# Optimization experiments

Hardware: AMD Instinct MI355X
Metric: run time of the kernel (lower is better)

## Reference

```python
import jax, jax.numpy as jnp
import numpy as np

OBS_DIM, GOAL_DIM, NUM_SKILLS, ACTION_DIM = 256, 64, 16, 32
HIDDEN = 128
BATCH = 65536


def setup_inputs() -> dict:
    key = jax.random.key(0)
    ks = jax.random.split(key, 10)
    s = lambda k, shape, fan_in: jax.random.normal(k, shape, jnp.float32) * (1.0 / np.sqrt(fan_in))
    return {
        "obs": jax.random.normal(ks[0], (BATCH, OBS_DIM), jnp.float32),
        "goals": jax.random.normal(ks[1], (BATCH, GOAL_DIM), jnp.float32),
        # gate (AlphaNet) params
        "Wa1": s(ks[2], (OBS_DIM + GOAL_DIM, HIDDEN), OBS_DIM + GOAL_DIM),
        "ba1": jnp.zeros((HIDDEN,), jnp.float32),
        "Wa2": s(ks[3], (HIDDEN, NUM_SKILLS), HIDDEN),
        "ba2": jnp.zeros((NUM_SKILLS,), jnp.float32),
        # stacked executor params: [S, in, out]
        "W1": s(ks[4], (NUM_SKILLS, OBS_DIM, HIDDEN), OBS_DIM),
        "b1": jnp.zeros((NUM_SKILLS, HIDDEN), jnp.float32),
        "W2": s(ks[5], (NUM_SKILLS, HIDDEN, ACTION_DIM), HIDDEN),
        "b2": jnp.zeros((NUM_SKILLS, ACTION_DIM), jnp.float32),
    }


def reference(obs, goals, Wa1, ba1, Wa2, ba2, W1, b1, W2, b2):
    # gate: softmax(Linear(ReLU(Linear(cat(obs, goals)))))
    concat_input = jnp.concatenate([obs, goals], axis=-1)  # [B, O+G]
    ha = jax.nn.relu(concat_input @ Wa1 + ba1)             # [B, H]
    alphas = jax.nn.softmax(ha @ Wa2 + ba2, axis=-1)       # [B, S]

    # all experts as one grouped GEMM over stacked weights
    h = jax.nn.relu(jnp.einsum("bo,soh->bsh", obs, W1) + b1[None])  # [B, S, H]
    skill_outputs = jnp.einsum("bsh,sha->bsa", h, W2) + b2[None]    # [B, S, A]

    # weighted sum over skills
    mixed_action = jnp.einsum("bsa,bs->ba", skill_outputs, alphas)  # [B, A]
    return mixed_action, alphas
```

## Files before the change

### kernel.cpp

```cpp
#include <hip/hip_runtime.h>


typedef __attribute__((ext_vector_type(8))) short    bf16x8;
typedef __attribute__((ext_vector_type(4))) float    f32x4;
typedef __attribute__((ext_vector_type(4))) _Float16 f16x4;
using half2v = decltype(__builtin_amdgcn_cvt_pkrtz(0.f, 0.f));

#define GATE_W1_OFF   0
#define GATE_W2_OFF   81920
#define GATE_BA1_OFF  86016
#define GATE_BA2_OFF  86528
#define GATE_BYTES    86592
#define S_W1_STRIDE   528
#define S_W2_OFF      67584
#define S_W2_STRIDE   272
#define S_B1_OFF      76288
#define S_B2_OFF      76800
#define S_IMG         76928
#define LDS_BYTES     163520

__device__ __forceinline__ unsigned short f2bf(float f) {
  unsigned u = __builtin_bit_cast(unsigned, f);
  return (unsigned short)((u + 0x7FFFu + ((u >> 16) & 1u)) >> 16);
}

__device__ __forceinline__ bf16x8 pack_bf8(f32x4 a, f32x4 b) {
  int4 r;
  asm("v_cvt_pk_bf16_f32 %0, %1, %2" : "=v"(r.x) : "v"(a[0]), "v"(a[1]));
  asm("v_cvt_pk_bf16_f32 %0, %1, %2" : "=v"(r.y) : "v"(a[2]), "v"(a[3]));
  asm("v_cvt_pk_bf16_f32 %0, %1, %2" : "=v"(r.z) : "v"(b[0]), "v"(b[1]));
  asm("v_cvt_pk_bf16_f32 %0, %1, %2" : "=v"(r.w) : "v"(b[2]), "v"(b[3]));
  return __builtin_bit_cast(bf16x8, r);
}

#define RELU_SCALE_PACK(dst, v, av, z)                                   \
  {                                                                      \
    half2v lo_ = __builtin_amdgcn_cvt_pkrtz((v)[0], (v)[1]);             \
    half2v hi_ = __builtin_amdgcn_cvt_pkrtz((v)[2], (v)[3]);             \
    lo_ = __builtin_elementwise_max(lo_, z) * (av);                      \
    hi_ = __builtin_elementwise_max(hi_, z) * (av);                      \
    dst[0] = (_Float16)lo_[0]; dst[1] = (_Float16)lo_[1];                \
    dst[2] = (_Float16)hi_[0]; dst[3] = (_Float16)hi_[1];                \
  }

__global__ void prep_weights(const float* __restrict__ Wa1, const float* __restrict__ Wa2,
                             const float* __restrict__ ba1, const float* __restrict__ ba2,
                             const float* __restrict__ W1,  const float* __restrict__ W2,
                             const float* __restrict__ b1,  const float* __restrict__ b2,
                             unsigned char* __restrict__ ws) {
  int i = blockIdx.x * 256 + threadIdx.x;
  if (i < 524288) {
    int s = i >> 15, r = i & 32767, h = r >> 8, o = r & 255;
    float v = W1[(s * 256 + o) * 128 + h];
    *(unsigned short*)(ws + GATE_BYTES + s * S_IMG + h * S_W1_STRIDE + 2 * o) = f2bf(v);
  } else if (i < 589824) {
    int j = i - 524288, s = j >> 12, r = j & 4095, a = r >> 7, h = r & 127;
    float v = W2[(s * 128 + h) * 32 + a];
    *(_Float16*)(ws + GATE_BYTES + s * S_IMG + S_W2_OFF + a * S_W2_STRIDE + 2 * h) =
        (_Float16)v;
  } else if (i < 630784) {
    int j = i - 589824, h = j / 320, o = j - h * 320;
    float v = Wa1[o * 128 + h];
    *(unsigned short*)(ws + GATE_W1_OFF + h * 640 +
                       ((2 * o) ^ ((h & 7) << 4))) = f2bf(v);
  } else if (i < 632832) {
    int j = i - 630784, n = j >> 7, h = j & 127;
    float v = Wa2[h * 16 + n];
    *(_Float16*)(ws + GATE_W2_OFF + n * 256 +
                 ((2 * h) ^ ((n & 7) << 3))) = (_Float16)v;
  } else if (i < 634880) {
    int j = i - 632832, s = j >> 7, h = j & 127;
    *(float*)(ws + GATE_BYTES + s * S_IMG + S_B1_OFF + 4 * h) = b1[s * 128 + h];
  } else if (i < 635392) {
    int j = i - 634880, s = j >> 5, a = j & 31;
    *(float*)(ws + GATE_BYTES + s * S_IMG + S_B2_OFF + 4 * a) = b2[s * 32 + a];
  } else if (i < 635520) {
    int j = i - 635392;
    *(float*)(ws + GATE_BA1_OFF + 4 * j) = ba1[j];
  } else if (i < 635536) {
    int j = i - 635520;
    *(float*)(ws + GATE_BA2_OFF + 4 * j) = ba2[j];
  }
}

__device__ __forceinline__ void stage_lin(const unsigned char* gsrc, unsigned char* ldst,
                                          int tid, int bytes) {
  for (int off = tid * 16; off < bytes; off += 512 * 16) {
    __builtin_amdgcn_global_load_lds(
        (const __attribute__((address_space(1))) unsigned int*)(const void*)(gsrc + off),
        (__attribute__((address_space(3))) unsigned int*)(void*)(ldst + off), 16, 0, 0);
  }
}

__global__ __launch_bounds__(512, 2)
void mop_fused(const float* __restrict__ obs, const float* __restrict__ goals,
               const unsigned char* __restrict__ ws, float* __restrict__ dout) {
  extern __shared__ unsigned char smem[];
  const int tid  = threadIdx.x;
  const int lane = tid & 63;
  const int wave = tid >> 6;
  const int l15  = lane & 15;
  const int g    = lane >> 4;
  const int swz4 = (lane & 7) << 4;
  const int swz3 = (lane & 7) << 3;
  const int rowbase = blockIdx.x * 256 + wave * 32;

  float* out_mixed = dout;
  float* out_alpha = dout + 65536 * 32;

  const int lw1 = l15 * S_W1_STRIDE + 16 * g;
  const int lw2 = S_W2_OFF + l15 * S_W2_STRIDE + 8 * g;
  const int lb  = 16 * g;

  stage_lin(ws, smem, tid, GATE_BYTES);

  bf16x8 obsf[2][8];
  bf16x8 goalf[2][2];
  #pragma unroll
  for (int nb = 0; nb < 2; ++nb) {
    const float* rp = obs + (size_t)(rowbase + nb * 16 + l15) * 256 + 8 * g;
    #pragma unroll
    for (int t = 0; t < 8; ++t) {
      f32x4 a = *(const f32x4*)(rp + 32 * t);
      f32x4 c = *(const f32x4*)(rp + 32 * t + 4);
      obsf[nb][t] = pack_bf8(a, c);
    }
    const float* gp = goals + (size_t)(rowbase + nb * 16 + l15) * 64 + 8 * g;
    #pragma unroll
    for (int t = 0; t < 2; ++t) {
      f32x4 a = *(const f32x4*)(gp + 32 * t);
      f32x4 c = *(const f32x4*)(gp + 32 * t + 4);
      goalf[nb][t] = pack_bf8(a, c);
    }
  }

  __syncthreads();

  stage_lin(ws + GATE_BYTES, smem + GATE_BYTES, tid, S_IMG);

  f32x4 gacc[2][8];
  #pragma unroll
  for (int ht = 0; ht < 8; ++ht) {
    f32x4 bias = *(const f32x4*)(smem + GATE_BA1_OFF + 64 * ht + lb);
    gacc[0][ht] = bias; gacc[1][ht] = bias;
  }
  #pragma unroll
  for (int t = 0; t < 10; ++t) {
    bf16x8 bf0 = (t < 8) ? obsf[0][t] : goalf[0][t - 8];
    bf16x8 bf1 = (t < 8) ? obsf[1][t] : goalf[1][t - 8];
    #pragma unroll
    for (int ht = 0; ht < 8; ++ht) {
      int row = 16 * ht + l15;
      bf16x8 af = *(const bf16x8*)(smem + GATE_W1_OFF + row * 640 +
                                   ((64 * t + 16 * g) ^ swz4));
      gacc[0][ht] = __builtin_amdgcn_mfma_f32_16x16x32_bf16(af, bf0, gacc[0][ht], 0, 0, 0);
      gacc[1][ht] = __builtin_amdgcn_mfma_f32_16x16x32_bf16(af, bf1, gacc[1][ht], 0, 0, 0);
    }
  }

  const half2v zh = __builtin_amdgcn_cvt_pkrtz(0.f, 0.f);
  f32x4 alph[2];
  #pragma unroll
  for (int nb = 0; nb < 2; ++nb) {
    f32x4 lacc = *(const f32x4*)(smem + GATE_BA2_OFF + lb);
    #pragma unroll
    for (int ht = 0; ht < 8; ++ht) {
      f32x4 v = gacc[nb][ht];
      f16x4 hf;
      {
        half2v lo_ = __builtin_amdgcn_cvt_pkrtz(v[0], v[1]);
        half2v hi_ = __builtin_amdgcn_cvt_pkrtz(v[2], v[3]);
        lo_ = __builtin_elementwise_max(lo_, zh);
        hi_ = __builtin_elementwise_max(hi_, zh);
        hf[0] = (_Float16)lo_[0]; hf[1] = (_Float16)lo_[1];
        hf[2] = (_Float16)hi_[0]; hf[3] = (_Float16)hi_[1];
      }
      f16x4 wf = *(const f16x4*)(smem + GATE_W2_OFF + l15 * 256 +
                                 ((32 * ht + 8 * g) ^ swz3));
      lacc = __builtin_amdgcn_mfma_f32_16x16x16f16(wf, hf, lacc, 0, 0, 0);
    }
    float m = fmaxf(fmaxf(lacc[0], lacc[1]), fmaxf(lacc[2], lacc[3]));
    m = fmaxf(m, __shfl_xor(m, 16, 64));
    m = fmaxf(m, __shfl_xor(m, 32, 64));
    f32x4 e;
    e[0] = __expf(lacc[0] - m); e[1] = __expf(lacc[1] - m);
    e[2] = __expf(lacc[2] - m); e[3] = __expf(lacc[3] - m);
    float ssum = e[0] + e[1] + e[2] + e[3];
    ssum += __shfl_xor(ssum, 16, 64);
    ssum += __shfl_xor(ssum, 32, 64);
    float inv = 1.0f / ssum;
    alph[nb] = e * inv;
    *(f32x4*)(out_alpha + (size_t)(rowbase + nb * 16 + l15) * 16 + 4 * g) = alph[nb];
  }

  __syncthreads();

  f32x4 macc[2][2] = {};
  for (int s = 0; s < 16; ++s) {
    const unsigned char* buf = smem + ((s & 1) ? 0 : GATE_BYTES);
    if (s < 15) {
      unsigned char* nbuf = smem + (((s + 1) & 1) ? 0 : GATE_BYTES);
      stage_lin(ws + GATE_BYTES + (size_t)(s + 1) * S_IMG, nbuf, tid, S_IMG);
    }
    f32x4 acc[2][8];
    #pragma unroll
    for (int ht = 0; ht < 8; ++ht) {
      f32x4 b1v = *(const f32x4*)(buf + S_B1_OFF + 64 * ht + lb);
      acc[0][ht] = b1v; acc[1][ht] = b1v;
    }

    const int asrc = ((s >> 2) << 4) | l15;
    float p0 = (s & 1) ? alph[0][1] : alph[0][0];
    float p1 = (s & 1) ? alph[0][3] : alph[0][2];
    float as0 = __shfl((s & 2) ? p1 : p0, asrc, 64);
    float q0 = (s & 1) ? alph[1][1] : alph[1][0];
    float q1 = (s & 1) ? alph[1][3] : alph[1][2];
    float as1 = __shfl((s & 2) ? q1 : q0, asrc, 64);
    const half2v a0h = __builtin_amdgcn_cvt_pkrtz(as0, as0);
    const half2v a1h = __builtin_amdgcn_cvt_pkrtz(as1, as1);

    const unsigned char* w1p = buf + lw1;
    const unsigned char* w2p = buf + lw2;

    __builtin_amdgcn_s_setprio(1);
    #pragma unroll
    for (int t = 0; t < 8; ++t) {
      const unsigned char* w1t = w1p + t * 64;
      #pragma unroll
      for (int ht = 0; ht < 8; ++ht) {
        bf16x8 af = *(const bf16x8*)(w1t + ht * 8448);
        acc[0][ht] = __builtin_amdgcn_mfma_f32_16x16x32_bf16(af, obsf[0][t], acc[0][ht], 0, 0, 0);
        acc[1][ht] = __builtin_amdgcn_mfma_f32_16x16x32_bf16(af, obsf[1][t], acc[1][ht], 0, 0, 0);
      }
    }
    #pragma unroll
    for (int ht = 0; ht < 8; ++ht) {
      f16x4 hf0, hf1;
      RELU_SCALE_PACK(hf0, acc[0][ht], a0h, zh);
      RELU_SCALE_PACK(hf1, acc[1][ht], a1h, zh);
      #pragma unroll
      for (int ta = 0; ta < 2; ++ta) {
        f16x4 wf = *(const f16x4*)(w2p + ta * 4352 + ht * 32);
        macc[0][ta] = __builtin_amdgcn_mfma_f32_16x16x16f16(wf, hf0, macc[0][ta], 0, 0, 0);
        macc[1][ta] = __builtin_amdgcn_mfma_f32_16x16x16f16(wf, hf1, macc[1][ta], 0, 0, 0);
      }
    }
    __builtin_amdgcn_s_setprio(0);
    #pragma unroll
    for (int ta = 0; ta < 2; ++ta) {
      f32x4 b2v = *(const f32x4*)(buf + S_B2_OFF + 64 * ta + lb);
      macc[0][ta] = macc[0][ta] + b2v * as0;
      macc[1][ta] = macc[1][ta] + b2v * as1;
    }
    __syncthreads();
  }

  #pragma unroll
  for (int nb = 0; nb < 2; ++nb) {
    #pragma unroll
    for (int ta = 0; ta < 2; ++ta) {
      *(f32x4*)(out_mixed + (size_t)(rowbase + nb * 16 + l15) * 32 + 16 * ta + 4 * g) =
          macc[nb][ta];
    }
  }
}

extern "C" void kernel_launch(void* const* d_in, const int* in_sizes, int n_in,
                              void* d_out, int out_size, void* d_ws, size_t ws_size,
                              hipStream_t stream) {
  const float* obs   = (const float*)d_in[0];
  const float* goals = (const float*)d_in[1];
  const float* Wa1   = (const float*)d_in[2];
  const float* ba1   = (const float*)d_in[3];
  const float* Wa2   = (const float*)d_in[4];
  const float* ba2   = (const float*)d_in[5];
  const float* W1    = (const float*)d_in[6];
  const float* b1    = (const float*)d_in[7];
  const float* W2    = (const float*)d_in[8];
  const float* b2    = (const float*)d_in[9];
  unsigned char* ws  = (unsigned char*)d_ws;
  float* out = (float*)d_out;

  prep_weights<<<2483, 256, 0, stream>>>(Wa1, Wa2, ba1, ba2, W1, W2, b1, b2, ws);
  mop_fused<<<256, 512, LDS_BYTES, stream>>>(obs, goals, ws, out);
}
```

Baseline: 93.70 us.

## Halve block to four waves, each computing 64 rows for more weight reuse

Result: slower. 117.3 us (+25.2%).

```diff
diff --git a/kernel.cpp b/kernel.cpp
--- a/kernel.cpp
+++ b/kernel.cpp
@@ -85,14 +85,14 @@
 
 __device__ __forceinline__ void stage_lin(const unsigned char* gsrc, unsigned char* ldst,
                                           int tid, int bytes) {
-  for (int off = tid * 16; off < bytes; off += 512 * 16) {
+  for (int off = tid * 16; off < bytes; off += 256 * 16) {
     __builtin_amdgcn_global_load_lds(
         (const __attribute__((address_space(1))) unsigned int*)(const void*)(gsrc + off),
         (__attribute__((address_space(3))) unsigned int*)(void*)(ldst + off), 16, 0, 0);
   }
 }
 
-__global__ __launch_bounds__(512, 2)
+__global__ __launch_bounds__(256, 1)
 void mop_fused(const float* __restrict__ obs, const float* __restrict__ goals,
                const unsigned char* __restrict__ ws, float* __restrict__ dout) {
   extern __shared__ unsigned char smem[];
@@ -103,7 +103,7 @@
   const int g    = lane >> 4;
   const int swz4 = (lane & 7) << 4;
   const int swz3 = (lane & 7) << 3;
-  const int rowbase = blockIdx.x * 256 + wave * 32;
+  const int rowbase = blockIdx.x * 256 + wave * 64;
 
   float* out_mixed = dout;
   float* out_alpha = dout + 65536 * 32;
@@ -114,10 +114,10 @@
 
   stage_lin(ws, smem, tid, GATE_BYTES);
 
-  bf16x8 obsf[2][8];
-  bf16x8 goalf[2][2];
-  #pragma unroll
-  for (int nb = 0; nb < 2; ++nb) {
+  bf16x8 obsf[4][8];
+  bf16x8 goalf[4][2];
+  #pragma unroll
+  for (int nb = 0; nb < 4; ++nb) {
     const float* rp = obs + (size_t)(rowbase + nb * 16 + l15) * 256 + 8 * g;
     #pragma unroll
     for (int t = 0; t < 8; ++t) {
@@ -138,30 +138,33 @@
 
   stage_lin(ws + GATE_BYTES, smem + GATE_BYTES, tid, S_IMG);
 
-  f32x4 gacc[2][8];
+  f32x4 gacc[4][8];
   #pragma unroll
   for (int ht = 0; ht < 8; ++ht) {
     f32x4 bias = *(const f32x4*)(smem + GATE_BA1_OFF + 64 * ht + lb);
-    gacc[0][ht] = bias; gacc[1][ht] = bias;
+    #pragma unroll
+    for (int nb = 0; nb < 4; ++nb) gacc[nb][ht] = bias;
   }
   #pragma unroll
   for (int t = 0; t < 10; ++t) {
-    bf16x8 bf0 = (t < 8) ? obsf[0][t] : goalf[0][t - 8];
-    bf16x8 bf1 = (t < 8) ? obsf[1][t] : goalf[1][t - 8];
+    bf16x8 bf[4];
+    #pragma unroll
+    for (int nb = 0; nb < 4; ++nb) bf[nb] = (t < 8) ? obsf[nb][t] : goalf[nb][t - 8];
     #pragma unroll
     for (int ht = 0; ht < 8; ++ht) {
       int row = 16 * ht + l15;
       bf16x8 af = *(const bf16x8*)(smem + GATE_W1_OFF + row * 640 +
                                    ((64 * t + 16 * g) ^ swz4));
-      gacc[0][ht] = __builtin_amdgcn_mfma_f32_16x16x32_bf16(af, bf0, gacc[0][ht], 0, 0, 0);
-      gacc[1][ht] = __builtin_amdgcn_mfma_f32_16x16x32_bf16(af, bf1, gacc[1][ht], 0, 0, 0);
+      #pragma unroll
+      for (int nb = 0; nb < 4; ++nb)
+        gacc[nb][ht] = __builtin_amdgcn_mfma_f32_16x16x32_bf16(af, bf[nb], gacc[nb][ht], 0, 0, 0);
     }
   }
 
   const half2v zh = __builtin_amdgcn_cvt_pkrtz(0.f, 0.f);
-  f32x4 alph[2];
-  #pragma unroll
-  for (int nb = 0; nb < 2; ++nb) {
+  f32x4 alph[4];
+  #pragma unroll
+  for (int nb = 0; nb < 4; ++nb) {
     f32x4 lacc = *(const f32x4*)(smem + GATE_BA2_OFF + lb);
     #pragma unroll
     for (int ht = 0; ht < 8; ++ht) {
@@ -195,29 +198,31 @@
 
   __syncthreads();
 
-  f32x4 macc[2][2] = {};
+  f32x4 macc[4][2] = {};
   for (int s = 0; s < 16; ++s) {
     const unsigned char* buf = smem + ((s & 1) ? 0 : GATE_BYTES);
     if (s < 15) {
       unsigned char* nbuf = smem + (((s + 1) & 1) ? 0 : GATE_BYTES);
       stage_lin(ws + GATE_BYTES + (size_t)(s + 1) * S_IMG, nbuf, tid, S_IMG);
     }
-    f32x4 acc[2][8];
+    f32x4 acc[4][8];
     #pragma unroll
     for (int ht = 0; ht < 8; ++ht) {
       f32x4 b1v = *(const f32x4*)(buf + S_B1_OFF + 64 * ht + lb);
-      acc[0][ht] = b1v; acc[1][ht] = b1v;
+      #pragma unroll
+      for (int nb = 0; nb < 4; ++nb) acc[nb][ht] = b1v;
     }
 
     const int asrc = ((s >> 2) << 4) | l15;
-    float p0 = (s & 1) ? alph[0][1] : alph[0][0];
-    float p1 = (s & 1) ? alph[0][3] : alph[0][2];
-    float as0 = __shfl((s & 2) ? p1 : p0, asrc, 64);
-    float q0 = (s & 1) ? alph[1][1] : alph[1][0];
-    float q1 = (s & 1) ? alph[1][3] : alph[1][2];
-    float as1 = __shfl((s & 2) ? q1 : q0, asrc, 64);
-    const half2v a0h = __builtin_amdgcn_cvt_pkrtz(as0, as0);
-    const half2v a1h = __builtin_amdgcn_cvt_pkrtz(as1, as1);
+    float av[4];
+    half2v ah[4];
+    #pragma unroll
+    for (int nb = 0; nb < 4; ++nb) {
+      float c0 = (s & 1) ? alph[nb][1] : alph[nb][0];
+      float c1 = (s & 1) ? alph[nb][3] : alph[nb][2];
+      av[nb] = __shfl((s & 2) ? c1 : c0, asrc, 64);
+      ah[nb] = __builtin_amdgcn_cvt_pkrtz(av[nb], av[nb]);
+    }
 
     const unsigned char* w1p = buf + lw1;
     const unsigned char* w2p = buf + lw2;
@@ -229,34 +234,37 @@
       #pragma unroll
       for (int ht = 0; ht < 8; ++ht) {
         bf16x8 af = *(const bf16x8*)(w1t + ht * 8448);
-        acc[0][ht] = __builtin_amdgcn_mfma_f32_16x16x32_bf16(af, obsf[0][t], acc[0][ht], 0, 0, 0);
-        acc[1][ht] = __builtin_amdgcn_mfma_f32_16x16x32_bf16(af, obsf[1][t], acc[1][ht], 0, 0, 0);
+        #pragma unroll
+        for (int nb = 0; nb < 4; ++nb)
+          acc[nb][ht] = __builtin_amdgcn_mfma_f32_16x16x32_bf16(af, obsf[nb][t], acc[nb][ht], 0, 0, 0);
       }
     }
     #pragma unroll
     for (int ht = 0; ht < 8; ++ht) {
-      f16x4 hf0, hf1;
-      RELU_SCALE_PACK(hf0, acc[0][ht], a0h, zh);
-      RELU_SCALE_PACK(hf1, acc[1][ht], a1h, zh);
+      f16x4 hf[4];
+      #pragma unroll
+      for (int nb = 0; nb < 4; ++nb) RELU_SCALE_PACK(hf[nb], acc[nb][ht], ah[nb], zh);
       #pragma unroll
       for (int ta = 0; ta < 2; ++ta) {
         f16x4 wf = *(const f16x4*)(w2p + ta * 4352 + ht * 32);
-        macc[0][ta] = __builtin_amdgcn_mfma_f32_16x16x16f16(wf, hf0, macc[0][ta], 0, 0, 0);
-        macc[1][ta] = __builtin_amdgcn_mfma_f32_16x16x16f16(wf, hf1, macc[1][ta], 0, 0, 0);
+        #pragma unroll
+        for (int nb = 0; nb < 4; ++nb)
+          macc[nb][ta] = __builtin_amdgcn_mfma_f32_16x16x16f16(wf, hf[nb], macc[nb][ta], 0, 0, 0);
       }
     }
     __builtin_amdgcn_s_setprio(0);
     #pragma unroll
     for (int ta = 0; ta < 2; ++ta) {
       f32x4 b2v = *(const f32x4*)(buf + S_B2_OFF + 64 * ta + lb);
-      macc[0][ta] = macc[0][ta] + b2v * as0;
-      macc[1][ta] = macc[1][ta] + b2v * as1;
+      #pragma unroll
+      for (int nb = 0; nb < 4; ++nb)
+        macc[nb][ta] = macc[nb][ta] + b2v * av[nb];
     }
     __syncthreads();
   }
 
   #pragma unroll
-  for (int nb = 0; nb < 2; ++nb) {
+  for (int nb = 0; nb < 4; ++nb) {
     #pragma unroll
     for (int ta = 0; ta < 2; ++ta) {
       *(f32x4*)(out_mixed + (size_t)(rowbase + nb * 16 + l15) * 32 + 16 * ta + 4 * g) =
@@ -282,5 +290,5 @@
   float* out = (float*)d_out;
 
   prep_weights<<<2483, 256, 0, stream>>>(Wa1, Wa2, ba1, ba2, W1, W2, b1, b2, ws);
-  mop_fused<<<256, 512, LDS_BYTES, stream>>>(obs, goals, ws, out);
-}
+  mop_fused<<<256, 256, LDS_BYTES, stream>>>(obs, goals, ws, out);
+}
```
